# Kernel tuning notes

Hardware: AMD Instinct MI355X
Metric: run time of the kernel (lower is better)

## Reference

```python
import jax, jax.numpy as jnp
import numpy as np

EPS = 1e-7


def ciou_pairwise(b1, b2):
    # b1: (N,1,4), b2: (1,N,4) in xyxy; returns (N,N) CIoU
    b1x1, b1y1, b1x2, b1y2 = b1[..., 0], b1[..., 1], b1[..., 2], b1[..., 3]
    b2x1, b2y1, b2x2, b2y2 = b2[..., 0], b2[..., 1], b2[..., 2], b2[..., 3]

    # intersection
    iw = jnp.clip(jnp.minimum(b1x2, b2x2) - jnp.maximum(b1x1, b2x1), 0.0)
    ih = jnp.clip(jnp.minimum(b1y2, b2y2) - jnp.maximum(b1y1, b2y1), 0.0)
    inter = iw * ih

    w1, h1 = b1x2 - b1x1, b1y2 - b1y1
    w2, h2 = b2x2 - b2x1, b2y2 - b2y1
    union = w1 * h1 + w2 * h2 - inter + EPS
    iou = inter / union

    # smallest enclosing box diagonal
    cw = jnp.maximum(b1x2, b2x2) - jnp.minimum(b1x1, b2x1)
    ch = jnp.maximum(b1y2, b2y2) - jnp.minimum(b1y1, b2y1)
    c2 = cw * cw + ch * ch + EPS

    # squared center distance
    rho2 = ((b2x1 + b2x2 - b1x1 - b1x2) ** 2 + (b2y1 + b2y2 - b1y1 - b1y2) ** 2) / 4.0

    # aspect-ratio consistency term
    v = (4.0 / (np.pi ** 2)) * (jnp.arctan(w2 / (h2 + EPS)) - jnp.arctan(w1 / (h1 + EPS))) ** 2
    alpha = jax.lax.stop_gradient(v / (v - iou + (1.0 + EPS)))
    return iou - (rho2 / c2 + v * alpha)


def setup_inputs() -> dict:
    key = jax.random.key(0)
    k1, k2, k3 = jax.random.split(key, 3)
    N = 4096
    conf = jax.random.uniform(k1, (N, 1), dtype=jnp.float32)           # confidence in [0,1)
    xy1 = jax.random.uniform(k2, (N, 2), dtype=jnp.float32) * 600.0    # top-left corner
    wh = jax.random.uniform(k3, (N, 2), dtype=jnp.float32) * 100.0 + 1.0  # width/height >= 1
    x = jnp.concatenate([conf, xy1, xy1 + wh], axis=1)                 # (N, 5): conf, x1, y1, x2, y2
    gamma = jnp.zeros((1,), dtype=jnp.float32)
    return {"x": x, "gamma": gamma}


def reference(x, gamma):
    boxes = x[:, 1:]
    conf = x[:, 0]
    iou = ciou_pairwise(boxes[:, None, :], boxes[None, :, :])          # (N, N)
    conf_matrix = conf[:, None] * conf[None, :]                        # (N, N) outer product
    attention = jax.nn.softmax(iou * conf_matrix, axis=-1)             # (N, N)
    x_prime = x * gamma + attention @ x                                # (N, 5)
    return jax.nn.sigmoid(x_prime)
```

## Files before the change

kernel.cpp:

```cpp
#include <hip/hip_runtime.h>
#include <math.h>

#define N 4096
#define FEPS 1e-7f
#define ROWS 4
#define BLK 256
#define JT 2
#define FSTRIDE 12

#define PART_OFF (N * FSTRIDE)


__global__ void precompute_kernel(const float* __restrict__ x, float* __restrict__ f) {
    int i = blockIdx.x * blockDim.x + threadIdx.x;
    if (i >= N) return;
    float cf = x[i * 5 + 0], x1 = x[i * 5 + 1], y1 = x[i * 5 + 2];
    float x2 = x[i * 5 + 3], y2 = x[i * 5 + 4];
    float w = x2 - x1, h = y2 - y1;
    float* fi = f + (size_t)i * FSTRIDE;
    fi[0] = cf; fi[1] = x1; fi[2] = y1; fi[3] = x2; fi[4] = y2;
    fi[5] = (x1 + x2) * 0.5f; fi[6] = (y1 + y2) * 0.5f; fi[7] = w; fi[8] = h;
    fi[9] = w * h + FEPS;
    fi[10] = 0.6366197723675814f * atanf(w / (h + FEPS));
    fi[11] = w * h;
}

__global__ __launch_bounds__(BLK) void ciou_attn_kernel(
        const float* __restrict__ f,
        float* __restrict__ part) {
    const int tid = threadIdx.x;
    const int g = blockIdx.x / JT;
    const int jt = blockIdx.x % JT;
    const int i0 = g * ROWS;

    float rx1[ROWS], ry1[ROWS], rx2[ROWS], ry2[ROWS], rsx[ROWS], rsy[ROWS];
    float rw[ROWS], rh[ROWS], rar[ROWS], rat[ROWS], rcf[ROWS];
#pragma unroll
    for (int r = 0; r < ROWS; r++) {
        const float* fi = f + (size_t)(i0 + r) * FSTRIDE;
        rcf[r] = fi[0]; rx1[r] = fi[1]; ry1[r] = fi[2]; rx2[r] = fi[3]; ry2[r] = fi[4];
        rsx[r] = fi[5]; rsy[r] = fi[6]; rw[r] = fi[7]; rh[r] = fi[8];
        rar[r] = fi[11]; rat[r] = fi[10];
    }

    float sum[ROWS];
    float acc[ROWS][5];
#pragma unroll
    for (int r = 0; r < ROWS; r++) {
        sum[r] = 0.f;
#pragma unroll
        for (int c = 0; c < 5; c++) acc[r][c] = 0.f;
    }

    const float ONEP = 1.f + FEPS;
    const int jend = (jt + 1) * (N / JT);

#pragma unroll 2
    for (int j = jt * (N / JT) + tid; j < jend; j += BLK) {
        const float4* fj = (const float4*)(f + (size_t)j * FSTRIDE);
        float4 A = fj[0], B = fj[1], C = fj[2];
        float jcf = A.x, jx1 = A.y, jy1 = A.z, jx2 = A.w;
        float jy2 = B.x, jsx = B.y, jsy = B.z, jw = B.w;
        float jh = C.x, jar2 = C.y, jat = C.z;
#pragma unroll
        for (int r = 0; r < ROWS; r++) {
            float iwr = fminf(rx2[r], jx2) - fmaxf(rx1[r], jx1);
            float ihr = fminf(ry2[r], jy2) - fmaxf(ry1[r], jy1);
            float iw = fmaxf(iwr, 0.f);
            float ih = fmaxf(ihr, 0.f);
            float inter = iw * ih;
            float uni = (rar[r] + jar2) - inter;
            float iou = fminf(inter * __builtin_amdgcn_rcpf(uni), 1.0f);
            float cw = (rw[r] + jw) - iwr;
            float ch = (rh[r] + jh) - ihr;
            float c2 = cw * cw + ch * ch + FEPS;
            float dx = jsx - rsx[r];
            float dy = jsy - rsy[r];
            float rho2 = dx * dx + dy * dy;
            float da = jat - rat[r];
            float v = da * da;
            float den = (v - iou) + ONEP;
            float valpha = v * v * __builtin_amdgcn_rcpf(den);
            float ciou = iou - (rho2 * __builtin_amdgcn_rcpf(c2) + valpha);
            float e = __expf(ciou * rcf[r] * jcf);
            sum[r] += e;
            acc[r][0] += e * jcf;
            acc[r][1] += e * jx1;
            acc[r][2] += e * jy1;
            acc[r][3] += e * jx2;
            acc[r][4] += e * jy2;
        }
    }

    __shared__ float red[BLK / 64][ROWS * 6];
    const int wave = tid >> 6;
    const int lane = tid & 63;
#pragma unroll
    for (int r = 0; r < ROWS; r++) {
        float v6[6] = {sum[r], acc[r][0], acc[r][1], acc[r][2], acc[r][3], acc[r][4]};
#pragma unroll
        for (int k = 0; k < 6; k++) {
            float val = v6[k];
#pragma unroll
            for (int off = 32; off > 0; off >>= 1) val += __shfl_down(val, off, 64);
            if (lane == 0) red[wave][r * 6 + k] = val;
        }
    }
    __syncthreads();
    if (tid < ROWS * 6) {
        float tot = 0.f;
#pragma unroll
        for (int w = 0; w < BLK / 64; w++) tot += red[w][tid];
        part[(size_t)blockIdx.x * (ROWS * 6) + tid] = tot;
    }
}

__global__ void epilogue_kernel(const float* __restrict__ x,
                                const float* __restrict__ gamma,
                                const float* __restrict__ part,
                                float* __restrict__ out) {
    int idx = blockIdx.x * blockDim.x + threadIdx.x;
    if (idx >= N * 5) return;
    int i = idx / 5, c = idx % 5;
    int g = i >> 2, r = i & 3;
    float se = 0.f, a = 0.f;
#pragma unroll
    for (int jt = 0; jt < JT; jt++) {
        const float* p = part + (size_t)(g * JT + jt) * (ROWS * 6) + r * 6;
        se += p[0];
        a += p[1 + c];
    }
    float xp = x[idx] * gamma[0] + a / se;
    out[idx] = 1.f / (1.f + expf(-xp));
}

extern "C" void kernel_launch(void* const* d_in, const int* in_sizes, int n_in,
                              void* d_out, int out_size, void* d_ws, size_t ws_size,
                              hipStream_t stream) {
    const float* x = (const float*)d_in[0];
    const float* gamma = (const float*)d_in[1];
    float* out = (float*)d_out;
    float* f = (float*)d_ws;
    float* part = (float*)d_ws + PART_OFF;

    precompute_kernel<<<(N + 255) / 256, 256, 0, stream>>>(x, f);
    ciou_attn_kernel<<<(N / ROWS) * JT, BLK, 0, stream>>>(f, part);
    epilogue_kernel<<<(N * 5 + 255) / 256, 256, 0, stream>>>(x, gamma, part, out);
}
```

Before: 88.19 us.

## Map one query row per thread with wave-uniform j loads and no reductions

Work is redistributed so that each thread owns one row i and loops over a 64-column chunk of j. Every lane reads the same j features (uniform, scalar-load friendly), which removes the cross-lane shuffle and shared-memory reductions. The epilogue now sums 64 partials per row instead of 2. The exp becomes exp2 with the log2(e) factor folded into a precomputed sqrt-scaled confidence, and the epsilon is split across the two per-box areas. The cost is a larger partial buffer (64*N*6 floats) and a heavier epilogue.

```diff
diff --git a/kernel.cpp b/kernel.cpp
--- a/kernel.cpp
+++ b/kernel.cpp
@@ -3,13 +3,13 @@
 
 #define N 4096
 #define FEPS 1e-7f
-#define ROWS 4
 #define BLK 256
-#define JT 2
+#define JT 64
+#define CH (N / JT)
 #define FSTRIDE 12
+#define N6 (N * 6)
 
 #define PART_OFF (N * FSTRIDE)
-
 
 __global__ void precompute_kernel(const float* __restrict__ x, float* __restrict__ f) {
     int i = blockIdx.x * blockDim.x + threadIdx.x;
@@ -20,99 +20,63 @@
     float* fi = f + (size_t)i * FSTRIDE;
     fi[0] = cf; fi[1] = x1; fi[2] = y1; fi[3] = x2; fi[4] = y2;
     fi[5] = (x1 + x2) * 0.5f; fi[6] = (y1 + y2) * 0.5f; fi[7] = w; fi[8] = h;
-    fi[9] = w * h + FEPS;
+    fi[9] = w * h + 0.5f * FEPS;
     fi[10] = 0.6366197723675814f * atanf(w / (h + FEPS));
-    fi[11] = w * h;
+    fi[11] = cf * 1.2011224087864498f;
 }
 
 __global__ __launch_bounds__(BLK) void ciou_attn_kernel(
         const float* __restrict__ f,
         float* __restrict__ part) {
-    const int tid = threadIdx.x;
-    const int g = blockIdx.x / JT;
+    const int gb = blockIdx.x / JT;
     const int jt = blockIdx.x % JT;
-    const int i0 = g * ROWS;
+    const int i = gb * BLK + threadIdx.x;
 
-    float rx1[ROWS], ry1[ROWS], rx2[ROWS], ry2[ROWS], rsx[ROWS], rsy[ROWS];
-    float rw[ROWS], rh[ROWS], rar[ROWS], rat[ROWS], rcf[ROWS];
-#pragma unroll
-    for (int r = 0; r < ROWS; r++) {
-        const float* fi = f + (size_t)(i0 + r) * FSTRIDE;
-        rcf[r] = fi[0]; rx1[r] = fi[1]; ry1[r] = fi[2]; rx2[r] = fi[3]; ry2[r] = fi[4];
-        rsx[r] = fi[5]; rsy[r] = fi[6]; rw[r] = fi[7]; rh[r] = fi[8];
-        rar[r] = fi[11]; rat[r] = fi[10];
+    const float4* fi = (const float4*)(f + (size_t)i * FSTRIDE);
+    float4 A = fi[0], B = fi[1], C = fi[2];
+    const float rx1 = A.y, ry1 = A.z, rx2 = A.w;
+    const float ry2 = B.x, rhx = B.y, rhy = B.z, rw = B.w;
+    const float rh = C.x, rareps = C.y, rat = C.z, rcf2 = C.w;
+
+    float sum = 0.f, a0 = 0.f, a1 = 0.f, a2 = 0.f, a3 = 0.f, a4 = 0.f;
+    const float ONEP = 1.f + FEPS;
+    const float* fj = f + (size_t)(jt * CH) * FSTRIDE;
+
+#pragma unroll 4
+    for (int jj = 0; jj < CH; jj++, fj += FSTRIDE) {
+        float jcf = fj[0], jx1 = fj[1], jy1 = fj[2], jx2 = fj[3], jy2 = fj[4];
+        float jhx = fj[5], jhy = fj[6], jw = fj[7], jh = fj[8];
+        float jareps = fj[9], jat = fj[10], jcf2 = fj[11];
+
+        float iwr = fminf(rx2, jx2) - fmaxf(rx1, jx1);
+        float ihr = fminf(ry2, jy2) - fmaxf(ry1, jy1);
+        float iw = fmaxf(iwr, 0.f);
+        float ih = fmaxf(ihr, 0.f);
+        float inter = iw * ih;
+        float uni = (rareps + jareps) - inter;
+        float iou = fminf(inter * __builtin_amdgcn_rcpf(uni), 1.0f);
+        float cw = (rw + jw) - iwr;
+        float ch = (rh + jh) - ihr;
+        float c2 = cw * cw + ch * ch + FEPS;
+        float dx = jhx - rhx;
+        float dy = jhy - rhy;
+        float rho2 = dx * dx + dy * dy;
+        float da = jat - rat;
+        float v = da * da;
+        float den = (v - iou) + ONEP;
+        float valpha = v * v * __builtin_amdgcn_rcpf(den);
+        float ciou = iou - (rho2 * __builtin_amdgcn_rcpf(c2) + valpha);
+        float e = __builtin_amdgcn_exp2f(ciou * (rcf2 * jcf2));
+        sum += e;
+        a0 += e * jcf;
+        a1 += e * jx1;
+        a2 += e * jy1;
+        a3 += e * jx2;
+        a4 += e * jy2;
     }
 
-    float sum[ROWS];
-    float acc[ROWS][5];
-#pragma unroll
-    for (int r = 0; r < ROWS; r++) {
-        sum[r] = 0.f;
-#pragma unroll
-        for (int c = 0; c < 5; c++) acc[r][c] = 0.f;
-    }
-
-    const float ONEP = 1.f + FEPS;
-    const int jend = (jt + 1) * (N / JT);
-
-#pragma unroll 2
-    for (int j = jt * (N / JT) + tid; j < jend; j += BLK) {
-        const float4* fj = (const float4*)(f + (size_t)j * FSTRIDE);
-        float4 A = fj[0], B = fj[1], C = fj[2];
-        float jcf = A.x, jx1 = A.y, jy1 = A.z, jx2 = A.w;
-        float jy2 = B.x, jsx = B.y, jsy = B.z, jw = B.w;
-        float jh = C.x, jar2 = C.y, jat = C.z;
-#pragma unroll
-        for (int r = 0; r < ROWS; r++) {
-            float iwr = fminf(rx2[r], jx2) - fmaxf(rx1[r], jx1);
-            float ihr = fminf(ry2[r], jy2) - fmaxf(ry1[r], jy1);
-            float iw = fmaxf(iwr, 0.f);
-            float ih = fmaxf(ihr, 0.f);
-            float inter = iw * ih;
-            float uni = (rar[r] + jar2) - inter;
-            float iou = fminf(inter * __builtin_amdgcn_rcpf(uni), 1.0f);
-            float cw = (rw[r] + jw) - iwr;
-            float ch = (rh[r] + jh) - ihr;
-            float c2 = cw * cw + ch * ch + FEPS;
-            float dx = jsx - rsx[r];
-            float dy = jsy - rsy[r];
-            float rho2 = dx * dx + dy * dy;
-            float da = jat - rat[r];
-            float v = da * da;
-            float den = (v - iou) + ONEP;
-            float valpha = v * v * __builtin_amdgcn_rcpf(den);
-            float ciou = iou - (rho2 * __builtin_amdgcn_rcpf(c2) + valpha);
-            float e = __expf(ciou * rcf[r] * jcf);
-            sum[r] += e;
-            acc[r][0] += e * jcf;
-            acc[r][1] += e * jx1;
-            acc[r][2] += e * jy1;
-            acc[r][3] += e * jx2;
-            acc[r][4] += e * jy2;
-        }
-    }
-
-    __shared__ float red[BLK / 64][ROWS * 6];
-    const int wave = tid >> 6;
-    const int lane = tid & 63;
-#pragma unroll
-    for (int r = 0; r < ROWS; r++) {
-        float v6[6] = {sum[r], acc[r][0], acc[r][1], acc[r][2], acc[r][3], acc[r][4]};
-#pragma unroll
-        for (int k = 0; k < 6; k++) {
-            float val = v6[k];
-#pragma unroll
-            for (int off = 32; off > 0; off >>= 1) val += __shfl_down(val, off, 64);
-            if (lane == 0) red[wave][r * 6 + k] = val;
-        }
-    }
-    __syncthreads();
-    if (tid < ROWS * 6) {
-        float tot = 0.f;
-#pragma unroll
-        for (int w = 0; w < BLK / 64; w++) tot += red[w][tid];
-        part[(size_t)blockIdx.x * (ROWS * 6) + tid] = tot;
-    }
+    float* p = part + (size_t)jt * N6 + (size_t)i * 6;
+    p[0] = sum; p[1] = a0; p[2] = a1; p[3] = a2; p[4] = a3; p[5] = a4;
 }
 
 __global__ void epilogue_kernel(const float* __restrict__ x,
@@ -122,13 +86,12 @@
     int idx = blockIdx.x * blockDim.x + threadIdx.x;
     if (idx >= N * 5) return;
     int i = idx / 5, c = idx % 5;
-    int g = i >> 2, r = i & 3;
     float se = 0.f, a = 0.f;
-#pragma unroll
+    const float* p = part + (size_t)i * 6;
+#pragma unroll 8
     for (int jt = 0; jt < JT; jt++) {
-        const float* p = part + (size_t)(g * JT + jt) * (ROWS * 6) + r * 6;
-        se += p[0];
-        a += p[1 + c];
+        se += p[jt * (size_t)N6 + 0];
+        a  += p[jt * (size_t)N6 + 1 + c];
     }
     float xp = x[idx] * gamma[0] + a / se;
     out[idx] = 1.f / (1.f + expf(-xp));
@@ -144,6 +107,6 @@
     float* part = (float*)d_ws + PART_OFF;
 
     precompute_kernel<<<(N + 255) / 256, 256, 0, stream>>>(x, f);
-    ciou_attn_kernel<<<(N / ROWS) * JT, BLK, 0, stream>>>(f, part);
+    ciou_attn_kernel<<<(N / BLK) * JT, BLK, 0, stream>>>(f, part);
     epilogue_kernel<<<(N * 5 + 255) / 256, 256, 0, stream>>>(x, gamma, part, out);
 }
```

New measurement: 87.77 us. About the same (-0.5%).
